# Kernel optimization log

Hardware: AMD Instinct MI355X
Metric: run time of the kernel (lower is better)

The kernel has to match this reference:

```python
import jax, jax.numpy as jnp
import numpy as np

B, T, D, H, NC, PS = 128, 256, 6, 512, 4, 12


def setup_inputs() -> dict:
    key = jax.random.key(0)
    ks = jax.random.split(key, 24)
    s = 1.0 / np.sqrt(H)
    u = lambda k, shape: jax.random.uniform(k, shape, jnp.float32, -s, s)
    inp = {
        'x': jax.random.normal(ks[0], (B, T, D), jnp.float32),
        # encoder LSTM (layer0 input D, layer1 input H); torch gate order i,f,g,o
        'enc_Wih0': u(ks[1], (4 * H, D)), 'enc_Whh0': u(ks[2], (4 * H, H)),
        'enc_bih0': u(ks[3], (4 * H,)),   'enc_bhh0': u(ks[4], (4 * H,)),
        'enc_Wih1': u(ks[5], (4 * H, H)), 'enc_Whh1': u(ks[6], (4 * H, H)),
        'enc_bih1': u(ks[7], (4 * H,)),   'enc_bhh1': u(ks[8], (4 * H,)),
        # decoder LSTM (both layers input H)
        'dec_Wih0': u(ks[9], (4 * H, H)),  'dec_Whh0': u(ks[10], (4 * H, H)),
        'dec_bih0': u(ks[11], (4 * H,)),   'dec_bhh0': u(ks[12], (4 * H,)),
        'dec_Wih1': u(ks[13], (4 * H, H)), 'dec_Whh1': u(ks[14], (4 * H, H)),
        'dec_bih1': u(ks[15], (4 * H,)),   'dec_bhh1': u(ks[16], (4 * H,)),
        # heads
        'fc_W': u(ks[17], (D, H)),  'fc_b': u(ks[18], (D,)),
        'cls_W': u(ks[19], (NC, H)), 'cls_b': u(ks[20], (NC,)),
        'reg_W': u(ks[21], (1, H)),  'reg_b': u(ks[22], (1,)),
    }
    return inp


def _cell(inp, h, c, Wih, Whh, bih, bhh):
    g = inp @ Wih.T + h @ Whh.T + bih + bhh  # [B,4H]
    i, f, gg, o = jnp.split(g, 4, axis=-1)
    c = jax.nn.sigmoid(f) * c + jax.nn.sigmoid(i) * jnp.tanh(gg)
    h = jax.nn.sigmoid(o) * jnp.tanh(c)
    return h, c


def _lstm_layer(x, Wih, Whh, bih, bhh):
    # x: [B,T,in] -> precompute input projections once: [T,B,4H]
    xg = jnp.einsum('bti,gi->tbg', x, Wih) + bih + bhh
    h0 = jnp.zeros((x.shape[0], H), x.dtype)
    c0 = jnp.zeros((x.shape[0], H), x.dtype)
    def step(carry, g_t):
        h, c = carry
        g = g_t + h @ Whh.T
        i, f, gg, o = jnp.split(g, 4, axis=-1)
        c = jax.nn.sigmoid(f) * c + jax.nn.sigmoid(i) * jnp.tanh(gg)
        h = jax.nn.sigmoid(o) * jnp.tanh(c)
        return (h, c), h
    (hT, cT), ys = jax.lax.scan(step, (h0, c0), xg)
    return jnp.transpose(ys, (1, 0, 2)), hT, cT  # [B,T,H]


def reference(x, enc_Wih0, enc_Whh0, enc_bih0, enc_bhh0,
              enc_Wih1, enc_Whh1, enc_bih1, enc_bhh1,
              dec_Wih0, dec_Whh0, dec_bih0, dec_bhh0,
              dec_Wih1, dec_Whh1, dec_bih1, dec_bhh1,
              fc_W, fc_b, cls_W, cls_b, reg_W, reg_b):
    out0, h0f, c0f = _lstm_layer(x, enc_Wih0, enc_Whh0, enc_bih0, enc_bhh0)
    out1, h1f, c1f = _lstm_layer(out0, enc_Wih1, enc_Whh1, enc_bih1, enc_bhh1)
    last = out1[:, -1, :]                      # [B,H]
    class_logits = last @ cls_W.T + cls_b      # [B,NC]
    time_regression = (last @ reg_W.T + reg_b)[:, 0]  # [B]
    def dstep(carry, _):
        h0, c0, h1, c1, inp = carry
        h0n, c0n = _cell(inp, h0, c0, dec_Wih0, dec_Whh0, dec_bih0, dec_bhh0)
        h1n, c1n = _cell(h0n, h1, c1, dec_Wih1, dec_Whh1, dec_bih1, dec_bhh1)
        pred = h1n @ fc_W.T + fc_b  # [B,D]
        return (h0n, c0n, h1n, c1n, h1n), pred
    init = (h0f, c0f, h1f, c1f, last)
    _, preds = jax.lax.scan(dstep, init, None, length=PS)  # [PS,B,D]
    forecast = jnp.transpose(preds, (1, 0, 2))             # [B,PS,D]
    return forecast, class_logits, time_regression
```

## Files before the change

kernel.cpp:

```cpp
#include <hip/hip_runtime.h>
#include <hip/hip_bf16.h>

typedef __attribute__((ext_vector_type(8))) short short8;
typedef __attribute__((ext_vector_type(4))) float floatx4;
typedef unsigned short u16;
typedef unsigned long long u64;

#define SCOPE_AGENT __HIP_MEMORY_SCOPE_AGENT


__device__ __forceinline__ u16 f2b(float f){
  union { float fl; unsigned u; } v; v.fl = f;
  unsigned r = v.u + 0x7fffu + ((v.u >> 16) & 1u);
  return (u16)(r >> 16);
}
__device__ __forceinline__ float b2f(u16 b){
  union { unsigned u; float f; } v; v.u = ((unsigned)b) << 16; return v.f;
}

__device__ __forceinline__ short8 ldc8(const u16* p){
  short8 r;
  asm volatile("global_load_dwordx4 %0, %1, off sc1" : "=&v"(r) : "v"(p));
  return r;
}
__device__ __forceinline__ void stc64(u64* p, u64 v){
  __hip_atomic_store(p, v, __ATOMIC_RELAXED, SCOPE_AGENT);
}

__device__ __forceinline__ bool expired(long long t0){
  return (wall_clock64() - t0) > 50000000LL;
}


__global__ void reorder_w_k(const float* __restrict__ W, u16* __restrict__ out){
  int idx = blockIdx.x*256 + threadIdx.x;
  int r = idx >> 9, k = idx & 511;
  int rp = ((r & 511) << 2) | (r >> 9);
  out[rp*512 + k] = f2b(W[idx]);
}
__global__ void prep_wx0_k(const float* __restrict__ W, u16* __restrict__ out){
  int idx = blockIdx.x*256 + threadIdx.x;
  int r = idx >> 5, k = idx & 31;
  int rp = ((r & 511) << 2) | (r >> 9);
  out[rp*32 + k] = (k < 6) ? f2b(W[r*6 + k]) : (u16)0;
}
__global__ void prep_bias_k(const float* __restrict__ bih, const float* __restrict__ bhh,
                            float* __restrict__ out){
  int r = blockIdx.x*256 + threadIdx.x;
  int rp = ((r & 511) << 2) | (r >> 9);
  out[rp] = bih[r] + bhh[r];
}
__global__ void prep_x_k(const float* __restrict__ x, u16* __restrict__ out){
  int idx = blockIdx.x*256 + threadIdx.x;
  int t = idx >> 12; int rem = idx & 4095; int b = rem >> 5; int k = rem & 31;
  out[idx] = (k < 6) ? f2b(x[(b*256 + t)*6 + k]) : (u16)0;
}
__global__ void init_out_k(float* __restrict__ out, const float* __restrict__ fcb,
                           const float* __restrict__ clsb, const float* __restrict__ regb){
  int i = blockIdx.x*256 + threadIdx.x;
  if (i < 9216)       out[i] = fcb[i % 6];
  else if (i < 9728)  out[i] = clsb[(i - 9216) & 3];
  else if (i < 9856)  out[i] = regb[0];
}


struct PK {
  const u16 *Xb, *Wx0, *W0hh, *W1ih, *W1hh, *Wd0ih, *Wd0hh, *Wd1ih, *Wd1hh;
  const float *Bs;
  u16 *h0b, *h1b;
  unsigned *F;
  const float *fcW, *clsW, *regW;
  float *out;
};

#define HB 65536

__device__ __forceinline__ void pollF(const unsigned* F, int bg, int thr0, int thr1,
                                      long long t0){
  const int lane = threadIdx.x & 63;
  const unsigned* ap = (lane < 32) ? (F + bg*32 + lane)
                                   : (F + 128 + bg*32 + (lane - 32));
  const int thr = (lane < 32) ? thr0 : thr1;
  for(;;){
    int v = (int)__hip_atomic_load(ap, __ATOMIC_RELAXED, SCOPE_AGENT);
    if (__all(v >= thr)) return;
    if (expired(t0)) return;
    if (__any((thr - v) > 2)) __builtin_amdgcn_s_sleep(16);
    else                      __builtin_amdgcn_s_sleep(1);
  }
}

template<int NK1, bool COH1>
__device__ __forceinline__ void lstm_step(
    const u16* __restrict__ A1, int a1rowlen, const u16* __restrict__ ldsW1, int st1,
    const u16* __restrict__ A2, const u16* __restrict__ ldsW2,
    const float* __restrict__ biasp, u16* __restrict__ hdst,
    float* creg, float (*g)[69], float* accX, float* hout,
    int bg, int nt, int wv, int kh, int lane)
{
  const int lrow = lane & 15, kq = lane >> 4;
  const int arow = bg*32 + wv*16 + lrow;
  constexpr int NA1 = (NK1 == 1) ? 1 : NK1/2;
  const int k1base = (NK1 == 1) ? 0 : kh*NA1;
  const bool hasA1 = (NK1 > 1) || (kh == 0);
  short8 a1[NA1], a2[8];
  {
    const u16* p1 = A1 + arow*a1rowlen + kq*8;
    if (hasA1){
      #pragma unroll
      for (int k = 0; k < NA1; ++k)
        a1[k] = COH1 ? ldc8(p1 + (k1base+k)*32) : *(const short8*)(p1 + (k1base+k)*32);
    }
    const u16* p2 = A2 + arow*512 + kq*8;
    #pragma unroll
    for (int k = 0; k < 8; ++k) a2[k] = ldc8(p2 + (kh*8+k)*32);
  }
  asm volatile("s_waitcnt vmcnt(0)" ::: "memory");
  __builtin_amdgcn_sched_barrier(0);
  floatx4 acc[4];
  #pragma unroll
  for (int nn = 0; nn < 4; ++nn) acc[nn] = (floatx4){0.f,0.f,0.f,0.f};
  if (hasA1){
    #pragma unroll
    for (int nn = 0; nn < 4; ++nn){
      const u16* wb = ldsW1 + (nn*16 + lrow)*st1 + kq*8;
      #pragma unroll
      for (int k = 0; k < NA1; ++k)
        acc[nn] = __builtin_amdgcn_mfma_f32_16x16x32_bf16(a1[k], *(const short8*)(wb + (k1base+k)*32), acc[nn], 0,0,0);
    }
  }
  #pragma unroll
  for (int nn = 0; nn < 4; ++nn){
    const u16* wb = ldsW2 + (nn*16 + lrow)*520 + kq*8;
    #pragma unroll
    for (int k = 0; k < 8; ++k)
      acc[nn] = __builtin_amdgcn_mfma_f32_16x16x32_bf16(a2[k], *(const short8*)(wb + (kh*8+k)*32), acc[nn], 0,0,0);
  }
  if (kh == 1){
    float* ax = accX + (wv*64 + lane)*16;
    #pragma unroll
    for (int nn = 0; nn < 4; ++nn)
      #pragma unroll
      for (int r = 0; r < 4; ++r) ax[nn*4 + r] = acc[nn][r];
  }
  __syncthreads();
  if (kh == 1) return;
  {
    const float* ax = accX + (wv*64 + lane)*16;
    #pragma unroll
    for (int nn = 0; nn < 4; ++nn)
      #pragma unroll
      for (int r = 0; r < 4; ++r) acc[nn][r] += ax[nn*4 + r];
  }
  #pragma unroll
  for (int nn = 0; nn < 4; ++nn){
    float bn = biasp[nn*16 + lrow];
    #pragma unroll
    for (int r = 0; r < 4; ++r)
      g[wv*16 + kq*4 + r][nn*16 + lrow] = acc[nn][r] + bn;
  }
  __builtin_amdgcn_wave_barrier();
  const int bl = lane >> 2, jq = lane & 3;
  const float* gr = g[wv*16 + bl];
  union { u16 h[4]; u64 q; } pk;
  #pragma unroll
  for (int jj = 0; jj < 4; ++jj){
    int cb = (jq*4 + jj)*4;
    float gi = gr[cb+0], gf = gr[cb+1], gg = gr[cb+2], go = gr[cb+3];
    float iv = 1.f/(1.f + expf(-gi));
    float fv = 1.f/(1.f + expf(-gf));
    float ov = 1.f/(1.f + expf(-go));
    float cn = fv*creg[jj] + iv*tanhf(gg);
    creg[jj] = cn;
    pk.h[jj] = f2b(ov * tanhf(cn));
    hout[jj] = b2f(pk.h[jj]);
  }
  stc64((u64*)(hdst + (bg*32 + wv*16 + bl)*512 + nt*16 + jq*4), pk.q);
}


__global__ __launch_bounds__(256, 1) __attribute__((amdgpu_waves_per_eu(1, 1)))
void persist_k(PK p){
  const int w = blockIdx.x, tid = threadIdx.x;
  const int wv2 = tid >> 6, lane = tid & 63;
  const int wv = wv2 & 1, kh = wv2 >> 1;
  const long long t0 = wall_clock64();
  __shared__ float g[32][69];
  __shared__ float accX[2*64*16];
  extern __shared__ u16 dynW[];
  unsigned* F = p.F;

  const int role = w >> 7;
  const int bg   = (w >> 5) & 3;
  const int nt   = w & 31;
  const int fidx = role*128 + bg*32 + nt;
  u16* WA = dynW;
  u16* WB = dynW + 64*520;
  float creg[4] = {0.f,0.f,0.f,0.f};
  float hout[4];

  auto setflag = [&](unsigned val){
    __syncthreads();
    if (tid == 0) __hip_atomic_store(F + fidx, val, __ATOMIC_RELAXED, SCOPE_AGENT);
  };

  if (role == 0){
    {
      const unsigned* sA = (const unsigned*)(p.Wx0 + nt*64*32);
      unsigned* dA = (unsigned*)WA;
      for (int i = tid; i < 64*16; i += 256){ int r = i>>4, c = i&15; dA[r*20+c] = sA[r*16+c]; }
      const unsigned* sB = (const unsigned*)(p.W0hh + (size_t)nt*64*512);
      unsigned* dB = (unsigned*)WB;
      for (int i = tid; i < 64*256; i += 256){ int r = i>>8, c = i&255; dB[r*260+c] = sB[r*256+c]; }
    }
    const float* biasp = p.Bs + nt*64;
    __syncthreads();
    for (int t = 0; t < 256; ++t){
      if (wv2 == 0) pollF(F, bg, t, t-3, t0);
      __syncthreads();
      lstm_step<1,false>(p.Xb + t*4096, 32, WA, 40,
                         p.h0b + ((t+3)&3)*HB, WB,
                         biasp, p.h0b + (t&3)*HB, creg, g, accX, hout, bg, nt, wv, kh, lane);
      setflag(t+1);
    }
    {
      const unsigned* sA = (const unsigned*)(p.Wd0ih + (size_t)nt*64*512);
      const unsigned* sB = (const unsigned*)(p.Wd0hh + (size_t)nt*64*512);
      unsigned* dA = (unsigned*)WA; unsigned* dB = (unsigned*)WB;
      for (int i = tid; i < 64*256; i += 256){
        int r = i>>8, c = i&255;
        dA[r*260+c] = sA[r*256+c]; dB[r*260+c] = sB[r*256+c];
      }
    }
    biasp = p.Bs + 4096 + nt*64;
    __syncthreads();
    for (int s = 0; s < 12; ++s){
      if (wv2 == 0) pollF(F, bg, 256+s, 256+s, t0);
      __syncthreads();
      lstm_step<16,true>(p.h1b + ((s+3)&3)*HB, 512, WA, 520,
                         p.h0b + ((s+3)&3)*HB, WB,
                         biasp, p.h0b + (s&3)*HB, creg, g, accX, hout, bg, nt, wv, kh, lane);
      setflag(257+s);
    }
  } else {
    {
      const unsigned* sA = (const unsigned*)(p.W1ih + (size_t)nt*64*512);
      const unsigned* sB = (const unsigned*)(p.W1hh + (size_t)nt*64*512);
      unsigned* dA = (unsigned*)WA; unsigned* dB = (unsigned*)WB;
      for (int i = tid; i < 64*256; i += 256){
        int r = i>>8, c = i&255;
        dA[r*260+c] = sA[r*256+c]; dB[r*260+c] = sB[r*256+c];
      }
    }
    const float* biasp = p.Bs + 2048 + nt*64;
    __syncthreads();
    const int batch = bg*32 + wv*16 + (lane >> 2);
    const int jq = lane & 3;
    for (int u = 0; u < 256; ++u){
      if (wv2 == 0) pollF(F, bg, u+1, u, t0);
      __syncthreads();
      lstm_step<16,true>(p.h0b + (u&3)*HB, 512, WA, 520,
                         p.h1b + ((u+3)&3)*HB, WB,
                         biasp, p.h1b + (u&3)*HB, creg, g, accX, hout, bg, nt, wv, kh, lane);
      if (u == 255 && kh == 0){
        float a[5] = {0.f,0.f,0.f,0.f,0.f};
        #pragma unroll
        for (int jj = 0; jj < 4; ++jj){
          int col = nt*16 + jq*4 + jj;
          float hv = hout[jj];
          a[0] += hv * p.clsW[col];
          a[1] += hv * p.clsW[512 + col];
          a[2] += hv * p.clsW[1024 + col];
          a[3] += hv * p.clsW[1536 + col];
          a[4] += hv * p.regW[col];
        }
        #pragma unroll
        for (int c = 0; c < 4; ++c) atomicAdd(&p.out[9216 + batch*4 + c], a[c]);
        atomicAdd(&p.out[9728 + batch], a[4]);
      }
      setflag(u+1);
    }
    {
      const unsigned* sA = (const unsigned*)(p.Wd1ih + (size_t)nt*64*512);
      const unsigned* sB = (const unsigned*)(p.Wd1hh + (size_t)nt*64*512);
      unsigned* dA = (unsigned*)WA; unsigned* dB = (unsigned*)WB;
      for (int i = tid; i < 64*256; i += 256){
        int r = i>>8, c = i&255;
        dA[r*260+c] = sA[r*256+c]; dB[r*260+c] = sB[r*256+c];
      }
    }
    biasp = p.Bs + 6144 + nt*64;
    __syncthreads();
    for (int s = 0; s < 12; ++s){
      if (wv2 == 0) pollF(F, bg, 257+s, 256+s, t0);
      __syncthreads();
      lstm_step<16,true>(p.h0b + (s&3)*HB, 512, WA, 520,
                         p.h1b + ((s+3)&3)*HB, WB,
                         biasp, p.h1b + (s&3)*HB, creg, g, accX, hout, bg, nt, wv, kh, lane);
      if (kh == 0){
        #pragma unroll
        for (int d = 0; d < 6; ++d){
          float ad = 0.f;
          #pragma unroll
          for (int jj = 0; jj < 4; ++jj)
            ad += hout[jj] * p.fcW[d*512 + nt*16 + jq*4 + jj];
          atomicAdd(&p.out[batch*72 + s*6 + d], ad);
        }
      }
      setflag(257+s);
    }
  }
}


extern "C" void kernel_launch(void* const* d_in, const int* in_sizes, int n_in,
                              void* d_out, int out_size, void* d_ws, size_t ws_size,
                              hipStream_t stream){
  const float* x     = (const float*)d_in[0];
  const float* eWih0 = (const float*)d_in[1];
  const float* eWhh0 = (const float*)d_in[2];
  const float* ebih0 = (const float*)d_in[3];
  const float* ebhh0 = (const float*)d_in[4];
  const float* eWih1 = (const float*)d_in[5];
  const float* eWhh1 = (const float*)d_in[6];
  const float* ebih1 = (const float*)d_in[7];
  const float* ebhh1 = (const float*)d_in[8];
  const float* dWih0 = (const float*)d_in[9];
  const float* dWhh0 = (const float*)d_in[10];
  const float* dbih0 = (const float*)d_in[11];
  const float* dbhh0 = (const float*)d_in[12];
  const float* dWih1 = (const float*)d_in[13];
  const float* dWhh1 = (const float*)d_in[14];
  const float* dbih1 = (const float*)d_in[15];
  const float* dbhh1 = (const float*)d_in[16];
  const float* fcW   = (const float*)d_in[17];
  const float* fcb   = (const float*)d_in[18];
  const float* clsW  = (const float*)d_in[19];
  const float* clsb  = (const float*)d_in[20];
  const float* regW  = (const float*)d_in[21];
  const float* regb  = (const float*)d_in[22];
  float* out = (float*)d_out;

  uintptr_t base = (uintptr_t)d_ws;
  auto carve = [&](size_t n)->void*{
    void* p = (void*)base; base += (n + 255) & ~(size_t)255; return p;
  };
  u16* Wx0b  = (u16*)carve(2048*32*2);
  u16* We0hh = (u16*)carve(2048*512*2);
  u16* We1ih = (u16*)carve(2048*512*2);
  u16* We1hh = (u16*)carve(2048*512*2);
  u16* Wd0ih = (u16*)carve(2048*512*2);
  u16* Wd0hh = (u16*)carve(2048*512*2);
  u16* Wd1ih = (u16*)carve(2048*512*2);
  u16* Wd1hh = (u16*)carve(2048*512*2);
  float* Bs  = (float*)carve(4*2048*4);
  u16* Xb    = (u16*)carve(256*128*32*2);
  u16* h0b   = (u16*)carve((size_t)4*HB*2);
  u16* h1b   = (u16*)carve((size_t)4*HB*2);
  unsigned* F = (unsigned*)carve(256*4);

  (void)hipMemsetAsync(h0b, 0, (size_t)4*HB*2 + (size_t)4*HB*2 + 1024, stream);

  reorder_w_k<<<4096,256,0,stream>>>(eWhh0, We0hh);
  reorder_w_k<<<4096,256,0,stream>>>(eWih1, We1ih);
  reorder_w_k<<<4096,256,0,stream>>>(eWhh1, We1hh);
  reorder_w_k<<<4096,256,0,stream>>>(dWih0, Wd0ih);
  reorder_w_k<<<4096,256,0,stream>>>(dWhh0, Wd0hh);
  reorder_w_k<<<4096,256,0,stream>>>(dWih1, Wd1ih);
  reorder_w_k<<<4096,256,0,stream>>>(dWhh1, Wd1hh);
  prep_wx0_k<<<256,256,0,stream>>>(eWih0, Wx0b);
  prep_bias_k<<<8,256,0,stream>>>(ebih0, ebhh0, Bs);
  prep_bias_k<<<8,256,0,stream>>>(ebih1, ebhh1, Bs + 2048);
  prep_bias_k<<<8,256,0,stream>>>(dbih0, dbhh0, Bs + 4096);
  prep_bias_k<<<8,256,0,stream>>>(dbih1, dbhh1, Bs + 6144);
  prep_x_k<<<4096,256,0,stream>>>(x, Xb);
  init_out_k<<<39,256,0,stream>>>(out, fcb, clsb, regb);

  PK p;
  p.Xb = Xb; p.Wx0 = Wx0b; p.W0hh = We0hh; p.W1ih = We1ih; p.W1hh = We1hh;
  p.Wd0ih = Wd0ih; p.Wd0hh = Wd0hh; p.Wd1ih = Wd1ih; p.Wd1hh = Wd1hh;
  p.Bs = Bs; p.h0b = h0b; p.h1b = h1b; p.F = F;
  p.fcW = fcW; p.clsW = clsW; p.regW = regW; p.out = out;

  const int dynLds = 2*64*520*2;
  (void)hipFuncSetAttribute((const void*)persist_k,
                            hipFuncAttributeMaxDynamicSharedMemorySize, dynLds);

  void* args[] = { &p };
  hipError_t e = hipLaunchCooperativeKernel((const void*)persist_k, dim3(256), dim3(256),
                                            args, dynLds, stream);
  if (e != hipSuccess){
    persist_k<<<dim3(256), dim3(256), dynLds, stream>>>(p);
  }
  (void)in_sizes; (void)n_in; (void)out_size; (void)ws_size;
}
```

Before: 2.186 ms.

## Split LSTM step K-reduction across four wave groups with 512-thread blocks

Doubles the block size to 512 threads so each gate tile's K dimension is split four ways instead of two. This shortens each wave's serial MFMA chain and global load batch inside every recurrent step. Three groups write their partial sums to LDS and the first group adds them up. The gate scratch buffer now reuses part of the partial-sum LDS region. The trade-off is extra LDS reduction traffic, a larger block barrier, and tighter register and occupancy limits.

New measurement: 2.221 ms. About the same (+1.6%).

```diff
diff --git a/kernel.cpp b/kernel.cpp
--- a/kernel.cpp
+++ b/kernel.cpp
@@ -95,15 +95,15 @@
     const u16* __restrict__ A1, int a1rowlen, const u16* __restrict__ ldsW1, int st1,
     const u16* __restrict__ A2, const u16* __restrict__ ldsW2,
     const float* __restrict__ biasp, u16* __restrict__ hdst,
-    float* creg, float (*g)[69], float* accX, float* hout,
-    int bg, int nt, int wv, int kh, int lane)
+    float* creg, float* accX, float* hout,
+    int bg, int nt, int wv, int kp, int lane)
 {
   const int lrow = lane & 15, kq = lane >> 4;
   const int arow = bg*32 + wv*16 + lrow;
-  constexpr int NA1 = (NK1 == 1) ? 1 : NK1/2;
-  const int k1base = (NK1 == 1) ? 0 : kh*NA1;
-  const bool hasA1 = (NK1 > 1) || (kh == 0);
-  short8 a1[NA1], a2[8];
+  constexpr int NA1 = (NK1 == 1) ? 1 : NK1/4;
+  const int k1base = (NK1 == 1) ? 0 : kp*NA1;
+  const bool hasA1 = (NK1 > 1) || (kp == 0);
+  short8 a1[NA1], a2[4];
   {
     const u16* p1 = A1 + arow*a1rowlen + kq*8;
     if (hasA1){
@@ -113,7 +113,7 @@
     }
     const u16* p2 = A2 + arow*512 + kq*8;
     #pragma unroll
-    for (int k = 0; k < 8; ++k) a2[k] = ldc8(p2 + (kh*8+k)*32);
+    for (int k = 0; k < 4; ++k) a2[k] = ldc8(p2 + (kp*4+k)*32);
   }
   asm volatile("s_waitcnt vmcnt(0)" ::: "memory");
   __builtin_amdgcn_sched_barrier(0);
@@ -133,35 +133,37 @@
   for (int nn = 0; nn < 4; ++nn){
     const u16* wb = ldsW2 + (nn*16 + lrow)*520 + kq*8;
     #pragma unroll
-    for (int k = 0; k < 8; ++k)
-      acc[nn] = __builtin_amdgcn_mfma_f32_16x16x32_bf16(a2[k], *(const short8*)(wb + (kh*8+k)*32), acc[nn], 0,0,0);
-  }
-  if (kh == 1){
-    float* ax = accX + (wv*64 + lane)*16;
+    for (int k = 0; k < 4; ++k)
+      acc[nn] = __builtin_amdgcn_mfma_f32_16x16x32_bf16(a2[k], *(const short8*)(wb + (kp*4+k)*32), acc[nn], 0,0,0);
+  }
+  if (kp > 0){
+    float* ax = accX + ((wv*3 + (kp-1))*64 + lane)*16;
     #pragma unroll
     for (int nn = 0; nn < 4; ++nn)
       #pragma unroll
       for (int r = 0; r < 4; ++r) ax[nn*4 + r] = acc[nn][r];
   }
   __syncthreads();
-  if (kh == 1) return;
-  {
-    const float* ax = accX + (wv*64 + lane)*16;
+  if (kp > 0) return;
+  #pragma unroll
+  for (int q = 0; q < 3; ++q){
+    const float* ax = accX + ((wv*3 + q)*64 + lane)*16;
     #pragma unroll
     for (int nn = 0; nn < 4; ++nn)
       #pragma unroll
       for (int r = 0; r < 4; ++r) acc[nn][r] += ax[nn*4 + r];
   }
+  float* gw = accX + wv*3*64*16;
   #pragma unroll
   for (int nn = 0; nn < 4; ++nn){
     float bn = biasp[nn*16 + lrow];
     #pragma unroll
     for (int r = 0; r < 4; ++r)
-      g[wv*16 + kq*4 + r][nn*16 + lrow] = acc[nn][r] + bn;
+      gw[(kq*4 + r)*69 + nn*16 + lrow] = acc[nn][r] + bn;
   }
   __builtin_amdgcn_wave_barrier();
   const int bl = lane >> 2, jq = lane & 3;
-  const float* gr = g[wv*16 + bl];
+  const float* gr = gw + bl*69;
   union { u16 h[4]; u64 q; } pk;
   #pragma unroll
   for (int jj = 0; jj < 4; ++jj){
@@ -179,14 +181,13 @@
 }
 
 
-__global__ __launch_bounds__(256, 1) __attribute__((amdgpu_waves_per_eu(1, 1)))
+__global__ __launch_bounds__(512, 1) __attribute__((amdgpu_waves_per_eu(1, 1)))
 void persist_k(PK p){
   const int w = blockIdx.x, tid = threadIdx.x;
   const int wv2 = tid >> 6, lane = tid & 63;
-  const int wv = wv2 & 1, kh = wv2 >> 1;
+  const int wv = wv2 & 1, kp = wv2 >> 1;
   const long long t0 = wall_clock64();
-  __shared__ float g[32][69];
-  __shared__ float accX[2*64*16];
+  __shared__ float accX[2*3*64*16];
   extern __shared__ u16 dynW[];
   unsigned* F = p.F;
 
@@ -208,10 +209,10 @@
     {
       const unsigned* sA = (const unsigned*)(p.Wx0 + nt*64*32);
       unsigned* dA = (unsigned*)WA;
-      for (int i = tid; i < 64*16; i += 256){ int r = i>>4, c = i&15; dA[r*20+c] = sA[r*16+c]; }
+      for (int i = tid; i < 64*16; i += 512){ int r = i>>4, c = i&15; dA[r*20+c] = sA[r*16+c]; }
       const unsigned* sB = (const unsigned*)(p.W0hh + (size_t)nt*64*512);
       unsigned* dB = (unsigned*)WB;
-      for (int i = tid; i < 64*256; i += 256){ int r = i>>8, c = i&255; dB[r*260+c] = sB[r*256+c]; }
+      for (int i = tid; i < 64*256; i += 512){ int r = i>>8, c = i&255; dB[r*260+c] = sB[r*256+c]; }
     }
     const float* biasp = p.Bs + nt*64;
     __syncthreads();
@@ -220,14 +221,14 @@
       __syncthreads();
       lstm_step<1,false>(p.Xb + t*4096, 32, WA, 40,
                          p.h0b + ((t+3)&3)*HB, WB,
-                         biasp, p.h0b + (t&3)*HB, creg, g, accX, hout, bg, nt, wv, kh, lane);
+                         biasp, p.h0b + (t&3)*HB, creg, accX, hout, bg, nt, wv, kp, lane);
       setflag(t+1);
     }
     {
       const unsigned* sA = (const unsigned*)(p.Wd0ih + (size_t)nt*64*512);
       const unsigned* sB = (const unsigned*)(p.Wd0hh + (size_t)nt*64*512);
       unsigned* dA = (unsigned*)WA; unsigned* dB = (unsigned*)WB;
-      for (int i = tid; i < 64*256; i += 256){
+      for (int i = tid; i < 64*256; i += 512){
         int r = i>>8, c = i&255;
         dA[r*260+c] = sA[r*256+c]; dB[r*260+c] = sB[r*256+c];
       }
@@ -239,7 +240,7 @@
       __syncthreads();
       lstm_step<16,true>(p.h1b + ((s+3)&3)*HB, 512, WA, 520,
                          p.h0b + ((s+3)&3)*HB, WB,
-                         biasp, p.h0b + (s&3)*HB, creg, g, accX, hout, bg, nt, wv, kh, lane);
+                         biasp, p.h0b + (s&3)*HB, creg, accX, hout, bg, nt, wv, kp, lane);
       setflag(257+s);
     }
   } else {
@@ -247,7 +248,7 @@
       const unsigned* sA = (const unsigned*)(p.W1ih + (size_t)nt*64*512);
       const unsigned* sB = (const unsigned*)(p.W1hh + (size_t)nt*64*512);
       unsigned* dA = (unsigned*)WA; unsigned* dB = (unsigned*)WB;
-      for (int i = tid; i < 64*256; i += 256){
+      for (int i = tid; i < 64*256; i += 512){
         int r = i>>8, c = i&255;
         dA[r*260+c] = sA[r*256+c]; dB[r*260+c] = sB[r*256+c];
       }
@@ -261,8 +262,8 @@
       __syncthreads();
       lstm_step<16,true>(p.h0b + (u&3)*HB, 512, WA, 520,
                          p.h1b + ((u+3)&3)*HB, WB,
-                         biasp, p.h1b + (u&3)*HB, creg, g, accX, hout, bg, nt, wv, kh, lane);
-      if (u == 255 && kh == 0){
+                         biasp, p.h1b + (u&3)*HB, creg, accX, hout, bg, nt, wv, kp, lane);
+      if (u == 255 && kp == 0){
         float a[5] = {0.f,0.f,0.f,0.f,0.f};
         #pragma unroll
         for (int jj = 0; jj < 4; ++jj){
@@ -284,7 +285,7 @@
       const unsigned* sA = (const unsigned*)(p.Wd1ih + (size_t)nt*64*512);
       const unsigned* sB = (const unsigned*)(p.Wd1hh + (size_t)nt*64*512);
       unsigned* dA = (unsigned*)WA; unsigned* dB = (unsigned*)WB;
-      for (int i = tid; i < 64*256; i += 256){
+      for (int i = tid; i < 64*256; i += 512){
         int r = i>>8, c = i&255;
         dA[r*260+c] = sA[r*256+c]; dB[r*260+c] = sB[r*256+c];
       }
@@ -296,8 +297,8 @@
       __syncthreads();
       lstm_step<16,true>(p.h0b + (s&3)*HB, 512, WA, 520,
                          p.h1b + ((s+3)&3)*HB, WB,
-                         biasp, p.h1b + (s&3)*HB, creg, g, accX, hout, bg, nt, wv, kh, lane);
-      if (kh == 0){
+                         biasp, p.h1b + (s&3)*HB, creg, accX, hout, bg, nt, wv, kp, lane);
+      if (kp == 0){
         #pragma unroll
         for (int d = 0; d < 6; ++d){
           float ad = 0.f;
@@ -387,10 +388,10 @@
                             hipFuncAttributeMaxDynamicSharedMemorySize, dynLds);
 
   void* args[] = { &p };
-  hipError_t e = hipLaunchCooperativeKernel((const void*)persist_k, dim3(256), dim3(256),
+  hipError_t e = hipLaunchCooperativeKernel((const void*)persist_k, dim3(256), dim3(512),
                                             args, dynLds, stream);
   if (e != hipSuccess){
-    persist_k<<<dim3(256), dim3(256), dynLds, stream>>>(p);
+    persist_k<<<dim3(256), dim3(512), dynLds, stream>>>(p);
   }
   (void)in_sizes; (void)n_in; (void)out_size; (void)ws_size;
 }
```
